# Performance work log

Measured on AMD Instinct MI355X. Metric: run time of the kernel, lower is better.

## Reference

```python
import jax, jax.numpy as jnp
import numpy as np
from jax import lax

# dims
B, H, W, C = 32, 64, 64, 256
FEATURES, HEADS, NQ = 256, 8, 2
K, STRIDE, PAD = 3, 2, 1
HD = FEATURES // HEADS  # head dim = 32


def setup_inputs() -> dict:
    key = jax.random.key(0)
    ks = jax.random.split(key, 7)
    x = jax.random.normal(ks[0], (B, H, W, C), jnp.float32)
    # learned shared queries: truncated normal * sqrt(1/head_dim)
    query = jax.random.truncated_normal(ks[1], -2.0, 2.0, (NQ, FEATURES), jnp.float32) * np.float32(np.sqrt(1.0 / HD))
    Wk = jax.random.normal(ks[2], (C, FEATURES), jnp.float32) * np.float32(np.sqrt(1.0 / C))  # lecun
    Wv = jax.random.normal(ks[3], (C, FEATURES), jnp.float32) * np.float32(np.sqrt(1.0 / C))
    rpe_bias = jax.random.truncated_normal(ks[4], -2.0, 2.0, (K * K, NQ * HEADS), jnp.float32) * np.float32(0.02)
    attn_scale_w = jax.random.normal(ks[5], (K * K, NQ * HEADS), jnp.float32) * np.float32(0.02)
    Wo = jax.random.normal(ks[6], (FEATURES, FEATURES), jnp.float32) * np.float32(np.sqrt(1.0 / FEATURES))
    return {"x": x, "query": query, "Wk": Wk, "Wv": Wv,
            "rpe_bias": rpe_bias, "attn_scale_w": attn_scale_w, "Wo": Wo}


def _qna_forward(x, query, Wk, Wv, rpe_bias, attn_scale_w, Wo):
    # --- queries: reshape to [NQ, HEADS, HD], unit-normalize per head, depth-scale ---
    q = query.reshape(NQ, HEADS, HD)
    q = q / (jnp.linalg.norm(q, axis=-1, keepdims=True) + 1e-6)
    q = q / jnp.sqrt(HD).astype(q.dtype)

    # --- fused QK: (q Wk^T) applied to x, never materializing per-window keys ---
    Wk_r = Wk.reshape(C, HEADS, HD)
    qWk = jnp.einsum('qHd,DHd->DqH', q, Wk_r)              # [C, NQ, HEADS]
    cost = jnp.einsum('bijD,DqH->bijqH', x, qWk)            # [B, H, W, NQ, HEADS]
    cost_exp = jnp.exp(cost - lax.stop_gradient(jnp.max(cost)))  # global shift, cancels in softmax

    # --- values ---
    v = jnp.einsum('bijD,DF->bijF', x, Wv)                  # [B, H, W, FEATURES]
    v_cost_exp = cost_exp[..., None] * v.reshape(B, H, W, 1, HEADS, HD)
    v_cost_exp = v_cost_exp.reshape(B, H, W, NQ * FEATURES)

    # --- relative position bias + per-offset query mixing scale ---
    rpe = rpe_bias.reshape(K, K, 1, NQ * HEADS)
    rpe_exp = jnp.exp(rpe - lax.stop_gradient(jnp.max(rpe)))  # shift cancels (appears in num & den)
    scale = attn_scale_w.reshape(K, K, 1, NQ * HEADS)
    num_kernel = jnp.repeat(rpe_exp * scale, HD, axis=-1)   # [K, K, 1, NQ*FEATURES]

    # numerator: windowed sum of exp(cost)*v weighted by exp(rpe)*scale (depthwise conv)
    num = lax.conv_general_dilated(
        v_cost_exp, num_kernel, window_strides=(STRIDE, STRIDE),
        padding=((PAD, PAD), (PAD, PAD)), feature_group_count=NQ * FEATURES,
        dimension_numbers=('NHWC', 'HWIO', 'NHWC'))
    # denominator: windowed sum of exp(cost) weighted by exp(rpe)
    den = lax.conv_general_dilated(
        cost_exp.reshape(B, H, W, NQ * HEADS), rpe_exp, window_strides=(STRIDE, STRIDE),
        padding=((PAD, PAD), (PAD, PAD)), feature_group_count=NQ * HEADS,
        dimension_numbers=('NHWC', 'HWIO', 'NHWC'))
    ho, wo = num.shape[1], num.shape[2]

    out = num.reshape(B, ho, wo, NQ, HEADS, HD) / den.reshape(B, ho, wo, NQ, HEADS, 1)
    out = out.sum(axis=3).reshape(B, ho, wo, FEATURES)      # combine queries
    return jnp.einsum('bijF,FO->bijO', out, Wo)             # output projection


def reference(x, query, Wk, Wv, rpe_bias, attn_scale_w, Wo):
    return _qna_forward(x, query, Wk, Wv, rpe_bias, attn_scale_w, Wo)
```

## Files before the change

### kernel.cpp

```cpp
#include <hip/hip_runtime.h>
#include <math.h>

typedef __attribute__((ext_vector_type(8))) short bf16x8;
typedef __attribute__((ext_vector_type(4))) float floatx4;

static __device__ __forceinline__ short f2bf(float f) {
    union { float f; unsigned u; } a; a.f = f;
    unsigned r = a.u + 0x7fffu + ((a.u >> 16) & 1u);
    return (short)(r >> 16);
}
static __device__ __forceinline__ float bf2f(short s) {
    union { unsigned u; float f; } c; c.u = ((unsigned)(unsigned short)s) << 16;
    return c.f;
}

__global__ __launch_bounds__(256) void prep_kernel(
    const float* __restrict__ query,
    const float* __restrict__ Wk,
    const float* __restrict__ rpe_bias,
    const float* __restrict__ attn_scale_w,
    const float* __restrict__ Wv,
    const float* __restrict__ Wo,
    float* __restrict__ rpe_exp,
    float* __restrict__ rpe_scale,
    short* __restrict__ Bq,
    short* __restrict__ Wvh,
    short* __restrict__ Bo)
{
    __shared__ float qn[16 * 33];
    __shared__ float Wt[16][260];
    __shared__ float qwk_s[16][17];
    int tid = threadIdx.x, bb = blockIdx.x;

    for (int i = tid; i < 512; i += 256) {
        int qq  = i >> 8;
        int rem = i & 255;
        int h   = rem >> 5;
        int d   = rem & 31;
        qn[((qq << 3) + h) * 33 + d] = query[i];
    }
    for (int i = tid; i < 16 * 256; i += 256)
        Wt[i >> 8][i & 255] = Wk[bb * 16 * 256 + i];
    __syncthreads();
    if (tid < 16) {
        float s = 0.f;
        #pragma unroll
        for (int d = 0; d < 32; ++d) { float t = qn[tid * 33 + d]; s += t * t; }
        float inv = 1.0f / ((sqrtf(s) + 1e-6f) * sqrtf(32.0f));
        #pragma unroll
        for (int d = 0; d < 32; ++d) qn[tid * 33 + d] *= inv;
    }
    __syncthreads();

    int g  = tid & 15;
    int Dl = tid >> 4;
    int h2 = g & 7;
    float acc = 0.f;
    #pragma unroll
    for (int d = 0; d < 32; ++d)
        acc += qn[g * 33 + d] * Wt[Dl][h2 * 32 + d];
    qwk_s[Dl][g] = acc;
    __syncthreads();

    {
        int kl = tid >> 4, gg = tid & 15;
        int k  = bb * 16 + kl;
        int kc = k >> 5, q5 = k & 31, qd = q5 >> 3, j = q5 & 7;
        int lane = qd * 16 + gg;
        Bq[kc * 512 + lane * 8 + j] = f2bf(qwk_s[kl][gg]);
    }

    for (int kl = 0; kl < 16; ++kl) {
        int k  = bb * 16 + kl;
        int kc = k >> 5, q5 = k & 31, qd = q5 >> 3, j = q5 & 7;
        int n  = tid;
        int gg = n & 15;
        int lane = qd * 16 + gg;
        float vv = Wv[k * 256 + n];
        float vo = Wo[k * 256 + n];
        int hh  = n >> 5, ntv = (n >> 4) & 1;
        Wvh[hh * 8192 + ntv * 4096 + kc * 512 + lane * 8 + j] = f2bf(vv);
        int nto = n >> 4;
        Bo[nto * 4096 + kc * 512 + lane * 8 + j] = f2bf(vo);
    }

    if (bb == 0 && tid < 144) {
        float r = expf(rpe_bias[tid]);
        rpe_exp[tid]   = r;
        rpe_scale[tid] = r * attn_scale_w[tid];
    }
}

#define XROW 264
#define CESROW 19
__global__ __launch_bounds__(512) void fused_kernel(
    const float* __restrict__ x,
    const float* __restrict__ rpe_exp,
    const float* __restrict__ rpe_scale,
    const short* __restrict__ Bq,
    const short* __restrict__ Wvh,
    const short* __restrict__ Bo,
    float* __restrict__ out)
{
    __shared__ short Xw[112 * XROW];
    __shared__ __align__(16) unsigned char pool[112 * CESROW * 4];
    __shared__ float wcoefs[8][9][16];
    __shared__ float invden[16][16];

    float* ces    = (float*)pool;
    short* out_tr = (short*)pool;

    int tid  = threadIdx.x;
    int lane = tid & 63, wv = tid >> 6;
    int m16  = lane & 15, quad = lane >> 4;

    int blk0 = blockIdx.x;
    int blk  = ((blk0 & 7) << 8) | (blk0 >> 3);
    int b   = blk >> 6;
    int io  = (blk >> 1) & 31;
    int hf  = blk & 1;
    int i0  = io * 2 - 1;
    int jbase = hf * 32 - 1;

    #pragma unroll
    for (int i = 0; i < 7; ++i) {
        int it  = tid + i * 512;
        int row = it >> 5;
        int l   = it & 31;
        int ky  = row / 34;
        int jloc = row - ky * 34;
        int ii = i0 + ky, jj = jbase + jloc;
        bool valid = (ky < 3) && (jloc < 33) &&
                     ((unsigned)ii < 64u) && ((unsigned)jj < 64u);
        bf16x8 s;
        if (valid) {
            const float* xp = x + ((size_t)(((b << 6) + ii) << 6) + jj) * 256 + l * 8;
            float4 f0 = *(const float4*)xp;
            float4 f1 = *(const float4*)(xp + 4);
            s[0] = f2bf(f0.x); s[1] = f2bf(f0.y); s[2] = f2bf(f0.z); s[3] = f2bf(f0.w);
            s[4] = f2bf(f1.x); s[5] = f2bf(f1.y); s[6] = f2bf(f1.z); s[7] = f2bf(f1.w);
        } else {
            #pragma unroll
            for (int j = 0; j < 8; ++j) s[j] = 0;
        }
        *(bf16x8*)&Xw[row * XROW + l * 8] = s;
    }
    __syncthreads();

    if (wv < 7) {
        floatx4 acc = (floatx4){0.f, 0.f, 0.f, 0.f};
        const short* bp = Bq + lane * 8;
        #pragma unroll
        for (int kc = 0; kc < 8; ++kc) {
            bf16x8 a  = *(const bf16x8*)&Xw[(wv * 16 + m16) * XROW + kc * 32 + quad * 8];
            bf16x8 bq = *(const bf16x8*)(bp + kc * 512);
            acc = __builtin_amdgcn_mfma_f32_16x16x32_bf16(a, bq, acc, 0, 0, 0);
        }
        #pragma unroll
        for (int r = 0; r < 4; ++r) {
            int p = wv * 16 + quad * 4 + r;
            int ky = p / 34, jloc = p - ky * 34;
            int ii = i0 + ky, jj = jbase + jloc;
            bool valid = (ky < 3) && (jloc < 33) &&
                         ((unsigned)ii < 64u) && ((unsigned)jj < 64u);
            ces[p * CESROW + m16] = valid ? expf(acc[r]) : 0.f;
        }
    }
    __syncthreads();

    if (tid < 256) {
        int op = tid >> 4, g = tid & 15;
        float den = 0.f;
        #pragma unroll
        for (int w = 0; w < 9; ++w) {
            int ky = w / 3, kx = w - ky * 3;
            int row = ky * 34 + 2 * op + kx;
            den = fmaf(rpe_exp[w * 16 + g], ces[row * CESROW + g], den);
        }
        invden[op][g] = 1.0f / den;
    }
    __syncthreads();

    for (int it = tid; it < 1152; it += 512) {
        int op = it / 72, r = it - op * 72;
        int w = r >> 3, h = r & 7;
        int ky = w / 3, kx = w - ky * 3;
        int row = ky * 34 + 2 * op + kx;
        wcoefs[h][w][op] =
            ces[row * CESROW + h]     * rpe_scale[w * 16 + h]     * invden[op][h] +
            ces[row * CESROW + 8 + h] * rpe_scale[w * 16 + 8 + h] * invden[op][8 + h];
    }
    __syncthreads();

    {
        int h = wv;
        float wc[9];
        #pragma unroll
        for (int w = 0; w < 9; ++w) wc[w] = wcoefs[h][w][m16];

        floatx4 acc0 = (floatx4){0.f, 0.f, 0.f, 0.f};
        floatx4 acc1 = (floatx4){0.f, 0.f, 0.f, 0.f};
        const short* bp    = Wvh + h * 8192 + lane * 8;
        const short* xbase = Xw + 2 * m16 * XROW + quad * 8;
        #pragma unroll
        for (int kc = 0; kc < 8; ++kc) {
            float z[8];
            #pragma unroll
            for (int j = 0; j < 8; ++j) z[j] = 0.f;
            #pragma unroll
            for (int w = 0; w < 9; ++w) {
                int ky = w / 3, kx = w - ky * 3;
                bf16x8 xv = *(const bf16x8*)(xbase + (ky * 34 + kx) * XROW + kc * 32);
                #pragma unroll
                for (int j = 0; j < 8; ++j)
                    z[j] = fmaf(wc[w], bf2f(xv[j]), z[j]);
            }
            bf16x8 a;
            #pragma unroll
            for (int j = 0; j < 8; ++j) a[j] = f2bf(z[j]);
            bf16x8 b0 = *(const bf16x8*)(bp + kc * 512);
            bf16x8 b1 = *(const bf16x8*)(bp + 4096 + kc * 512);
            acc0 = __builtin_amdgcn_mfma_f32_16x16x32_bf16(a, b0, acc0, 0, 0, 0);
            acc1 = __builtin_amdgcn_mfma_f32_16x16x32_bf16(a, b1, acc1, 0, 0, 0);
        }
        #pragma unroll
        for (int r = 0; r < 4; ++r) {
            out_tr[(quad * 4 + r) * XROW + h * 32 + m16]      = f2bf(acc0[r]);
            out_tr[(quad * 4 + r) * XROW + h * 32 + 16 + m16] = f2bf(acc1[r]);
        }
    }
    __syncthreads();

    {
        floatx4 acc0 = (floatx4){0.f, 0.f, 0.f, 0.f};
        floatx4 acc1 = (floatx4){0.f, 0.f, 0.f, 0.f};
        int nt0 = wv * 2;
        const short* bp = Bo + nt0 * 4096 + lane * 8;
        #pragma unroll
        for (int kc = 0; kc < 8; ++kc) {
            bf16x8 a  = *(const bf16x8*)&out_tr[m16 * XROW + kc * 32 + quad * 8];
            bf16x8 b0 = *(const bf16x8*)(bp + kc * 512);
            bf16x8 b1 = *(const bf16x8*)(bp + 4096 + kc * 512);
            acc0 = __builtin_amdgcn_mfma_f32_16x16x32_bf16(a, b0, acc0, 0, 0, 0);
            acc1 = __builtin_amdgcn_mfma_f32_16x16x32_bf16(a, b1, acc1, 0, 0, 0);
        }
        size_t op0 = (size_t)blk * 16;
        #pragma unroll
        for (int r = 0; r < 4; ++r) {
            out[(op0 + quad * 4 + r) * 256 + nt0 * 16 + m16]       = acc0[r];
            out[(op0 + quad * 4 + r) * 256 + (nt0 + 1) * 16 + m16] = acc1[r];
        }
    }
}

extern "C" void kernel_launch(void* const* d_in, const int* in_sizes, int n_in,
                              void* d_out, int out_size, void* d_ws, size_t ws_size,
                              hipStream_t stream)
{
    const float* x     = (const float*)d_in[0];
    const float* query = (const float*)d_in[1];
    const float* Wk    = (const float*)d_in[2];
    const float* Wv    = (const float*)d_in[3];
    const float* rpe   = (const float*)d_in[4];
    const float* asw   = (const float*)d_in[5];
    const float* Wo    = (const float*)d_in[6];
    float* out = (float*)d_out;

    float* ws        = (float*)d_ws;
    float* rpe_exp   = ws;
    float* rpe_scale = ws + 144;
    short* Bq        = (short*)(ws + 288);
    short* Wvh       = (short*)(ws + 288 + 2048);
    short* Bo        = (short*)(ws + 288 + 2048 + 32768);

    prep_kernel<<<dim3(16), dim3(256), 0, stream>>>(query, Wk, rpe, asw, Wv, Wo,
                                                    rpe_exp, rpe_scale, Bq, Wvh, Bo);
    fused_kernel<<<dim3(2048), dim3(512), 0, stream>>>(x, rpe_exp, rpe_scale,
                                                       Bq, Wvh, Bo, out);
}
```

Baseline: 258.1 us.

## Compute V projection per window pixel, then weighted-sum values instead of inputs

Reorders the value path. Before, each head's wave formed per-output weighted sums of x over the 9 window taps (one 256-wide sum per head), then projected with Wv. Now the 7 waves project all 112 window pixels through the full Wv into the LDS x buffer, and a scalar pass applies the 9-tap per-head weights to the projected values. This removes the 8x redundant per-head 9-tap accumulation over 256 channels. In exchange it adds a 112x256x256 MFMA GEMM per block (versus 16x256x256 before) and an extra bf16 rounding of the projected values, and it reuses the Xw buffer for the result.

```diff
diff --git a/kernel.cpp b/kernel.cpp
--- a/kernel.cpp
+++ b/kernel.cpp
@@ -78,10 +78,9 @@
         int lane = qd * 16 + gg;
         float vv = Wv[k * 256 + n];
         float vo = Wo[k * 256 + n];
-        int hh  = n >> 5, ntv = (n >> 4) & 1;
-        Wvh[hh * 8192 + ntv * 4096 + kc * 512 + lane * 8 + j] = f2bf(vv);
-        int nto = n >> 4;
-        Bo[nto * 4096 + kc * 512 + lane * 8 + j] = f2bf(vo);
+        int nt  = n >> 4;
+        Wvh[nt * 4096 + kc * 512 + lane * 8 + j] = f2bf(vv);
+        Bo[nt * 4096 + kc * 512 + lane * 8 + j]  = f2bf(vo);
     }
 
     if (bb == 0 && tid < 144) {
@@ -148,14 +147,18 @@
     __syncthreads();
 
     if (wv < 7) {
-        floatx4 acc = (floatx4){0.f, 0.f, 0.f, 0.f};
-        const short* bp = Bq + lane * 8;
-        #pragma unroll
-        for (int kc = 0; kc < 8; ++kc) {
-            bf16x8 a  = *(const bf16x8*)&Xw[(wv * 16 + m16) * XROW + kc * 32 + quad * 8];
-            bf16x8 bq = *(const bf16x8*)(bp + kc * 512);
-            acc = __builtin_amdgcn_mfma_f32_16x16x32_bf16(a, bq, acc, 0, 0, 0);
-        }
+        bf16x8 Arow[8];
+        const short* xrow = &Xw[(wv * 16 + m16) * XROW + quad * 8];
+        #pragma unroll
+        for (int kc = 0; kc < 8; ++kc)
+            Arow[kc] = *(const bf16x8*)(xrow + kc * 32);
+
+        floatx4 accc = (floatx4){0.f, 0.f, 0.f, 0.f};
+        const short* bq = Bq + lane * 8;
+        #pragma unroll
+        for (int kc = 0; kc < 8; ++kc)
+            accc = __builtin_amdgcn_mfma_f32_16x16x32_bf16(
+                       Arow[kc], *(const bf16x8*)(bq + kc * 512), accc, 0, 0, 0);
         #pragma unroll
         for (int r = 0; r < 4; ++r) {
             int p = wv * 16 + quad * 4 + r;
@@ -163,7 +166,27 @@
             int ii = i0 + ky, jj = jbase + jloc;
             bool valid = (ky < 3) && (jloc < 33) &&
                          ((unsigned)ii < 64u) && ((unsigned)jj < 64u);
-            ces[p * CESROW + m16] = valid ? expf(acc[r]) : 0.f;
+            ces[p * CESROW + m16] = valid ? expf(accc[r]) : 0.f;
+        }
+
+        const short* bv = Wvh + lane * 8;
+        #pragma unroll
+        for (int ntp = 0; ntp < 8; ++ntp) {
+            floatx4 a0 = (floatx4){0.f, 0.f, 0.f, 0.f};
+            floatx4 a1 = (floatx4){0.f, 0.f, 0.f, 0.f};
+            const short* bp0 = bv + (2 * ntp) * 4096;
+            #pragma unroll
+            for (int kc = 0; kc < 8; ++kc) {
+                bf16x8 b0 = *(const bf16x8*)(bp0 + kc * 512);
+                bf16x8 b1 = *(const bf16x8*)(bp0 + 4096 + kc * 512);
+                a0 = __builtin_amdgcn_mfma_f32_16x16x32_bf16(Arow[kc], b0, a0, 0, 0, 0);
+                a1 = __builtin_amdgcn_mfma_f32_16x16x32_bf16(Arow[kc], b1, a1, 0, 0, 0);
+            }
+            #pragma unroll
+            for (int r = 0; r < 4; ++r) {
+                Xw[(wv * 16 + quad * 4 + r) * XROW + ntp * 32 + m16]      = f2bf(a0[r]);
+                Xw[(wv * 16 + quad * 4 + r) * XROW + ntp * 32 + 16 + m16] = f2bf(a1[r]);
+            }
         }
     }
     __syncthreads();
@@ -193,41 +216,30 @@
     __syncthreads();
 
     {
-        int h = wv;
-        float wc[9];
-        #pragma unroll
-        for (int w = 0; w < 9; ++w) wc[w] = wcoefs[h][w][m16];
-
-        floatx4 acc0 = (floatx4){0.f, 0.f, 0.f, 0.f};
-        floatx4 acc1 = (floatx4){0.f, 0.f, 0.f, 0.f};
-        const short* bp    = Wvh + h * 8192 + lane * 8;
-        const short* xbase = Xw + 2 * m16 * XROW + quad * 8;
-        #pragma unroll
-        for (int kc = 0; kc < 8; ++kc) {
-            float z[8];
-            #pragma unroll
-            for (int j = 0; j < 8; ++j) z[j] = 0.f;
-            #pragma unroll
-            for (int w = 0; w < 9; ++w) {
-                int ky = w / 3, kx = w - ky * 3;
-                bf16x8 xv = *(const bf16x8*)(xbase + (ky * 34 + kx) * XROW + kc * 32);
-                #pragma unroll
-                for (int j = 0; j < 8; ++j)
-                    z[j] = fmaf(wc[w], bf2f(xv[j]), z[j]);
-            }
-            bf16x8 a;
-            #pragma unroll
-            for (int j = 0; j < 8; ++j) a[j] = f2bf(z[j]);
-            bf16x8 b0 = *(const bf16x8*)(bp + kc * 512);
-            bf16x8 b1 = *(const bf16x8*)(bp + 4096 + kc * 512);
-            acc0 = __builtin_amdgcn_mfma_f32_16x16x32_bf16(a, b0, acc0, 0, 0, 0);
-            acc1 = __builtin_amdgcn_mfma_f32_16x16x32_bf16(a, b1, acc1, 0, 0, 0);
-        }
-        #pragma unroll
-        for (int r = 0; r < 4; ++r) {
-            out_tr[(quad * 4 + r) * XROW + h * 32 + m16]      = f2bf(acc0[r]);
-            out_tr[(quad * 4 + r) * XROW + h * 32 + 16 + m16] = f2bf(acc1[r]);
-        }
+        int op = tid >> 5;
+        int nc = tid & 31;
+        int n0 = nc * 8;
+        int h  = nc >> 2;
+        float wcv[9];
+        #pragma unroll
+        for (int w = 0; w < 9; ++w) wcv[w] = wcoefs[h][w][op];
+
+        float o[8];
+        #pragma unroll
+        for (int j = 0; j < 8; ++j) o[j] = 0.f;
+        #pragma unroll
+        for (int w = 0; w < 9; ++w) {
+            int ky = w / 3, kx = w - ky * 3;
+            int row = ky * 34 + 2 * op + kx;
+            bf16x8 vv = *(const bf16x8*)&Xw[row * XROW + n0];
+            #pragma unroll
+            for (int j = 0; j < 8; ++j)
+                o[j] = fmaf(wcv[w], bf2f(vv[j]), o[j]);
+        }
+        bf16x8 ob;
+        #pragma unroll
+        for (int j = 0; j < 8; ++j) ob[j] = f2bf(o[j]);
+        *(bf16x8*)&out_tr[op * XROW + n0] = ob;
     }
     __syncthreads();
 
```

After: 306.6 us. +18.8%, slower.
